# Optimization experiments

Measured on AMD Instinct MI355X. Metric: run time of the kernel, lower is better.

## Reference

```python
import jax, jax.numpy as jnp
import numpy as np

N_NODES = 50000
N_EDGES = 800000
DIM = 128
LAYERS = 3


def setup_inputs() -> dict:
    key = jax.random.key(0)
    k1, k2, k3, k4 = jax.random.split(key, 4)
    x = jax.random.normal(k1, (N_NODES, DIM), dtype=jnp.float32)
    edge_index = jax.random.randint(k2, (2, N_EDGES), 0, N_NODES, dtype=jnp.int64)
    scale = 1.0 / np.sqrt(DIM)
    W_rel = jax.random.normal(k3, (LAYERS, DIM, DIM), dtype=jnp.float32) * scale
    W_root = jax.random.normal(k4, (LAYERS, DIM, DIM), dtype=jnp.float32) * scale
    b = jnp.zeros((LAYERS, DIM), dtype=jnp.float32)
    return {"x": x, "edge_index": edge_index, "W_rel": W_rel, "W_root": W_root, "b": b}


def graph_conv(x, src, dst, w_rel, w_root, bias):
    # message: gather source node features along each edge  [E, D]
    msg = x[src]
    # add-aggregation per destination node                  [N, D]
    agg = jax.ops.segment_sum(msg, dst, num_segments=N_NODES)
    # out_i = W_rel @ agg_i + W_root @ x_i + b
    return agg @ w_rel + x @ w_root + bias


def reference(x, edge_index, W_rel, W_root, b):
    src, dst = edge_index[0], edge_index[1]
    for l in range(LAYERS):
        x = graph_conv(x, src, dst, W_rel[l], W_root[l], b[l])
    return x
```

## Files before the change

kernel.cpp:

```cpp
#include <hip/hip_runtime.h>

#define N_NODES 50000
#define N_EDGES 800000
#define DIM     128
#define LAYERS  3

#define BSHIFT    7
#define N_BUCKETS 391
#define CHUNK     4096
#define N_CHUNKS  196

using short8 = __attribute__((ext_vector_type(8))) short;
using f32x4  = __attribute__((ext_vector_type(4))) float;

__device__ __forceinline__ unsigned short f2bf(float f) {
    unsigned int u = __builtin_bit_cast(unsigned int, f);
    unsigned int r = (u + 0x7fffu + ((u >> 16) & 1u)) >> 16;
    return (unsigned short)r;
}
__device__ __forceinline__ float bfl(unsigned int u) {
    return __builtin_bit_cast(float, u << 16);
}
__device__ __forceinline__ float bfh(unsigned int u) {
    return __builtin_bit_cast(float, u & 0xffff0000u);
}


__global__ __launch_bounds__(256) void convert_x(const float* __restrict__ x,
                                                 unsigned short* __restrict__ xb) {
    int t = blockIdx.x * 256 + threadIdx.x;
    size_t base = (size_t)t * 8;
    if (base >= (size_t)N_NODES * DIM) return;
    float4 v0 = *(const float4*)(x + base);
    float4 v1 = *(const float4*)(x + base + 4);
    uint4 o;
    o.x = ((unsigned)f2bf(v0.y) << 16) | f2bf(v0.x);
    o.y = ((unsigned)f2bf(v0.w) << 16) | f2bf(v0.z);
    o.z = ((unsigned)f2bf(v1.y) << 16) | f2bf(v1.x);
    o.w = ((unsigned)f2bf(v1.w) << 16) | f2bf(v1.z);
    *(uint4*)(xb + base) = o;
}

__global__ __launch_bounds__(256) void prep_w(const float* __restrict__ Wrel,
                                              const float* __restrict__ Wroot,
                                              unsigned short* __restrict__ Wt) {
    int t = blockIdx.x * 256 + threadIdx.x;
    if (t >= LAYERS * 2 * 128 * 32) return;
    int k4  = t & 31;
    int col = (t >> 5) & 127;
    int mat = (t >> 12) & 1;
    int l   = t >> 13;
    const float* W = (mat ? Wroot : Wrel) + (size_t)l * DIM * DIM;
    int k0 = k4 * 4;
    unsigned short b0 = f2bf(W[(size_t)(k0 + 0) * DIM + col]);
    unsigned short b1 = f2bf(W[(size_t)(k0 + 1) * DIM + col]);
    unsigned short b2 = f2bf(W[(size_t)(k0 + 2) * DIM + col]);
    unsigned short b3 = f2bf(W[(size_t)(k0 + 3) * DIM + col]);
    uint2 o;
    o.x = ((unsigned)b1 << 16) | b0;
    o.y = ((unsigned)b3 << 16) | b2;
    *(uint2*)(Wt + (size_t)l * 128 * 256 + (size_t)col * 256 + mat * 128 + k0) = o;
}


__global__ __launch_bounds__(1024) void bin_count(const int* __restrict__ dst,
                                                  int* __restrict__ bcnt) {
    __shared__ int hist[N_BUCKETS];
    int tid = threadIdx.x, chunk = blockIdx.x;
    for (int t = tid; t < N_BUCKETS; t += 1024) hist[t] = 0;
    __syncthreads();
    int base = chunk * CHUNK;
#pragma unroll
    for (int i = 0; i < CHUNK; i += 1024) {
        int e = base + i + tid;
        if (e < N_EDGES) atomicAdd(&hist[dst[e] >> BSHIFT], 1);
    }
    __syncthreads();
    for (int t = tid; t < N_BUCKETS; t += 1024)
        bcnt[chunk * N_BUCKETS + t] = hist[t];
}

__global__ __launch_bounds__(512) void bscan(const int* __restrict__ bcnt,
                                             int* __restrict__ boff,
                                             int* __restrict__ bucket_start) {
    __shared__ int sh[512];
    int b = threadIdx.x;
    int run = 0;
    if (b < N_BUCKETS) {
        for (int c = 0; c < N_CHUNKS; ++c) {
            int v = bcnt[c * N_BUCKETS + b];
            boff[c * N_BUCKETS + b] = run;
            run += v;
        }
    }
    sh[b] = (b < N_BUCKETS) ? run : 0;
    __syncthreads();
    for (int off = 1; off < 512; off <<= 1) {
        int t = (b >= off) ? sh[b - off] : 0;
        __syncthreads();
        sh[b] += t;
        __syncthreads();
    }
    if (b < N_BUCKETS) bucket_start[b] = sh[b] - run;
    if (b == N_BUCKETS - 1) bucket_start[N_BUCKETS] = sh[b];
}

__global__ __launch_bounds__(1024) void bin_scatter(const int* __restrict__ src,
                                                    const int* __restrict__ dst,
                                                    const int* __restrict__ bucket_start,
                                                    const int* __restrict__ boff,
                                                    unsigned int* __restrict__ pairs) {
    __shared__ int cur[N_BUCKETS];
    int tid = threadIdx.x, chunk = blockIdx.x;
    for (int t = tid; t < N_BUCKETS; t += 1024)
        cur[t] = bucket_start[t] + boff[chunk * N_BUCKETS + t];
    __syncthreads();
    int base = chunk * CHUNK;
#pragma unroll
    for (int i = 0; i < CHUNK; i += 1024) {
        int e = base + i + tid;
        if (e < N_EDGES) {
            int d = dst[e];
            int b = d >> BSHIFT;
            int p = atomicAdd(&cur[b], 1);
            pairs[p] = ((unsigned)(d & 127) << 16) | (unsigned)src[e];
        }
    }
}

__global__ __launch_bounds__(1024) void fill_lds(const unsigned int* __restrict__ pairs,
                                                 const int* __restrict__ bucket_start,
                                                 int* __restrict__ row_start,
                                                 unsigned short* __restrict__ srcs16) {
    __shared__ int hist[128];
    __shared__ int offs[128];
    __shared__ int cur[128];
    __shared__ unsigned short srt[4096];
    int b = blockIdx.x, tid = threadIdx.x;
    int s0 = bucket_start[b], s1 = bucket_start[b + 1];
    int cnt = s1 - s0;
    if (tid < 128) hist[tid] = 0;
    __syncthreads();
    for (int k = tid; k < cnt; k += 1024)
        atomicAdd(&hist[pairs[s0 + k] >> 16], 1);
    __syncthreads();
    if (tid < 128) offs[tid] = hist[tid];
    __syncthreads();
    for (int off = 1; off < 128; off <<= 1) {
        int t = 0;
        if (tid < 128 && tid >= off) t = offs[tid - off];
        __syncthreads();
        if (tid < 128) offs[tid] += t;
        __syncthreads();
    }
    if (tid < 128) {
        int excl = offs[tid] - hist[tid];
        cur[tid] = excl;
        int node = b * 128 + tid;
        if (node <= N_NODES) row_start[node] = s0 + excl;
    }
    __syncthreads();
    for (int k = tid; k < cnt; k += 1024) {
        unsigned int u = pairs[s0 + k];
        int p = atomicAdd(&cur[u >> 16], 1);
        srt[p] = (unsigned short)(u & 0xffffu);
    }
    __syncthreads();
    for (int k = tid; k < cnt; k += 1024)
        srcs16[s0 + k] = srt[k];
}


__device__ __forceinline__ void acc8(float* a, uint4 v) {
    a[0] += bfl(v.x); a[1] += bfh(v.x);
    a[2] += bfl(v.y); a[3] += bfh(v.y);
    a[4] += bfl(v.z); a[5] += bfh(v.z);
    a[6] += bfl(v.w); a[7] += bfh(v.w);
}

__global__ __launch_bounds__(256) void aggregate_bf16(const unsigned short* __restrict__ xb,
                                                      const int* __restrict__ row_start,
                                                      const unsigned short* __restrict__ srcs,
                                                      unsigned short* __restrict__ aggb) {
    int tid  = threadIdx.x;
    int L    = tid & 15;
    int node = blockIdx.x * 16 + (tid >> 4);
    if (node >= N_NODES) return;
    int j   = row_start[node];
    int end = row_start[node + 1];

    const uint4* xq = (const uint4*)xb;
    float a[8] = {0.f, 0.f, 0.f, 0.f, 0.f, 0.f, 0.f, 0.f};

    for (; j + 7 < end; j += 8) {
        uint4 v0 = xq[(size_t)srcs[j]     * 16 + L];
        uint4 v1 = xq[(size_t)srcs[j + 1] * 16 + L];
        uint4 v2 = xq[(size_t)srcs[j + 2] * 16 + L];
        uint4 v3 = xq[(size_t)srcs[j + 3] * 16 + L];
        uint4 v4 = xq[(size_t)srcs[j + 4] * 16 + L];
        uint4 v5 = xq[(size_t)srcs[j + 5] * 16 + L];
        uint4 v6 = xq[(size_t)srcs[j + 6] * 16 + L];
        uint4 v7 = xq[(size_t)srcs[j + 7] * 16 + L];
        acc8(a, v0); acc8(a, v1); acc8(a, v2); acc8(a, v3);
        acc8(a, v4); acc8(a, v5); acc8(a, v6); acc8(a, v7);
    }
    if (j + 3 < end) {
        uint4 v0 = xq[(size_t)srcs[j]     * 16 + L];
        uint4 v1 = xq[(size_t)srcs[j + 1] * 16 + L];
        uint4 v2 = xq[(size_t)srcs[j + 2] * 16 + L];
        uint4 v3 = xq[(size_t)srcs[j + 3] * 16 + L];
        acc8(a, v0); acc8(a, v1); acc8(a, v2); acc8(a, v3);
        j += 4;
    }
    int rem = end - j;
    if (rem > 0) {
        int j1 = (rem > 1) ? j + 1 : j;
        int j2 = (rem > 2) ? j + 2 : j;
        uint4 v0 = xq[(size_t)srcs[j]  * 16 + L];
        uint4 v1 = xq[(size_t)srcs[j1] * 16 + L];
        uint4 v2 = xq[(size_t)srcs[j2] * 16 + L];
        acc8(a, v0);
        if (rem > 1) acc8(a, v1);
        if (rem > 2) acc8(a, v2);
    }

    uint4 o;
    o.x = ((unsigned)f2bf(a[1]) << 16) | f2bf(a[0]);
    o.y = ((unsigned)f2bf(a[3]) << 16) | f2bf(a[2]);
    o.z = ((unsigned)f2bf(a[5]) << 16) | f2bf(a[4]);
    o.w = ((unsigned)f2bf(a[7]) << 16) | f2bf(a[6]);
    ((uint4*)aggb)[(size_t)node * 16 + L] = o;
}


__global__ __launch_bounds__(256) void gemm_bf16(const unsigned short* __restrict__ aggb,
                                                 const unsigned short* __restrict__ xb,
                                                 const unsigned short* __restrict__ Wt_l,
                                                 const float* __restrict__ bias,
                                                 unsigned short* __restrict__ outb,
                                                 float* __restrict__ outf) {
    __shared__ unsigned short Bs[128 * 256];

    int tid  = threadIdx.x;
    int lane = tid & 63;
    int w    = tid >> 6;

#pragma unroll
    for (int i = 0; i < 16; ++i) {
        int c   = tid + i * 256;
        int col = c >> 5;
        int q   = c & 31;
        uint4 v = ((const uint4*)Wt_l)[c];
        *(uint4*)&Bs[col * 256 + 8 * (q ^ (col & 7))] = v;
    }
    __syncthreads();

    int row0 = blockIdx.x * 128 + w * 32;

    f32x4 acc[2][8];
#pragma unroll
    for (int m = 0; m < 2; ++m)
#pragma unroll
        for (int n = 0; n < 8; ++n) acc[m][n] = (f32x4){0.f, 0.f, 0.f, 0.f};

    const short8 zero8 = {0, 0, 0, 0, 0, 0, 0, 0};

#pragma unroll
    for (int ch = 0; ch < 8; ++ch) {
        const unsigned short* Asrc = (ch < 4) ? aggb : xb;
        int k0 = (ch & 3) * 32 + (lane >> 4) * 8;

        short8 a[2];
#pragma unroll
        for (int m = 0; m < 2; ++m) {
            int r = row0 + m * 16 + (lane & 15);
            a[m] = (r < N_NODES) ? *(const short8*)(Asrc + (size_t)r * DIM + k0) : zero8;
        }

        int qbase = ch * 4 + (lane >> 4);
#pragma unroll
        for (int n = 0; n < 8; ++n) {
            int col = n * 16 + (lane & 15);
            short8 b = *(const short8*)&Bs[col * 256 + 8 * (qbase ^ (col & 7))];
            acc[0][n] = __builtin_amdgcn_mfma_f32_16x16x32_bf16(a[0], b, acc[0][n], 0, 0, 0);
            acc[1][n] = __builtin_amdgcn_mfma_f32_16x16x32_bf16(a[1], b, acc[1][n], 0, 0, 0);
        }
    }

#pragma unroll
    for (int n = 0; n < 8; ++n) {
        int col = n * 16 + (lane & 15);
        float bv = bias[col];
#pragma unroll
        for (int m = 0; m < 2; ++m) {
            int rb = row0 + m * 16 + (lane >> 4) * 4;
#pragma unroll
            for (int r = 0; r < 4; ++r) {
                int row = rb + r;
                if (row < N_NODES) {
                    float v = acc[m][n][r] + bv;
                    if (outf) outf[(size_t)row * DIM + col] = v;
                    else      outb[(size_t)row * DIM + col] = f2bf(v);
                }
            }
        }
    }
}


extern "C" void kernel_launch(void* const* d_in, const int* in_sizes, int n_in,
                              void* d_out, int out_size, void* d_ws, size_t ws_size,
                              hipStream_t stream) {
    const float* x0    = (const float*)d_in[0];
    const int*   ei    = (const int*)d_in[1];
    const float* Wrel  = (const float*)d_in[2];
    const float* Wroot = (const float*)d_in[3];
    const float* bvec  = (const float*)d_in[4];
    float* out = (float*)d_out;

    char* ws = (char*)d_ws;
    const size_t XB = (size_t)N_NODES * DIM * sizeof(unsigned short);
    unsigned short* xbA  = (unsigned short*)ws;
    unsigned short* xbB  = (unsigned short*)(ws + XB);
    unsigned short* aggb = (unsigned short*)(ws + 2 * XB);
    unsigned int* pairs  = (unsigned int*)(ws + 2 * XB);
    int* bcnt            = (int*)(ws + 2 * XB + 3200000);
    int* boff            = (int*)(ws + 2 * XB + 3506944);
    int* bucket_start    = (int*)(ws + 2 * XB + 3813504);
    unsigned short* Wt   = (unsigned short*)(ws + 3 * XB);
    unsigned short* srcs16 = (unsigned short*)(ws + 3 * XB + 196608);
    int* row_start       = (int*)(ws + 3 * XB + 196608 + 1600000);

    const int* src = ei;
    const int* dst = ei + N_EDGES;

    convert_x<<<(N_NODES * DIM / 8 + 255) / 256, 256, 0, stream>>>(x0, xbA);
    prep_w<<<(LAYERS * 2 * 128 * 32 + 255) / 256, 256, 0, stream>>>(Wrel, Wroot, Wt);

    bin_count<<<N_CHUNKS, 1024, 0, stream>>>(dst, bcnt);
    bscan<<<1, 512, 0, stream>>>(bcnt, boff, bucket_start);
    bin_scatter<<<N_CHUNKS, 1024, 0, stream>>>(src, dst, bucket_start, boff, pairs);
    fill_lds<<<N_BUCKETS, 1024, 0, stream>>>(pairs, bucket_start, row_start, srcs16);

    unsigned short* xin = xbA;
    unsigned short* xouts[LAYERS] = {xbB, xbA, nullptr};
    for (int l = 0; l < LAYERS; ++l) {
        aggregate_bf16<<<(N_NODES + 15) / 16, 256, 0, stream>>>(xin, row_start, srcs16, aggb);
        gemm_bf16<<<(N_NODES + 127) / 128, 256, 0, stream>>>(
            aggb, xin, Wt + (size_t)l * 128 * 256, bvec + (size_t)l * DIM,
            xouts[l], (l == LAYERS - 1) ? out : nullptr);
        xin = xouts[l];
    }
}
```

Measured before the change: 243.6 us.

## Fuse neighbor aggregation and GEMM into one per-layer kernel

Merges the aggregate and GEMM kernels into a single kernel per layer. Each block of 64 nodes gathers neighbor sums into LDS and then runs MFMA directly from LDS, which removes the global write and re-read of the aggregated buffer and one launch per layer. Weights are pre-packed in MFMA fragment order and read straight from global/L2 instead of being staged in LDS. The trade-offs are lower per-block GEMM reuse (64 rows instead of 128), per-wave weight reloads from cache, and the block's MFMA phase waiting on its slowest node's gather.

Result: no change. 240.4 us (-1.3%).

```diff
diff --git a/kernel.cpp b/kernel.cpp
--- a/kernel.cpp
+++ b/kernel.cpp
@@ -9,6 +9,8 @@
 #define N_BUCKETS 391
 #define CHUNK     4096
 #define N_CHUNKS  196
+
+#define AS_STRIDE 136
 
 using short8 = __attribute__((ext_vector_type(8))) short;
 using f32x4  = __attribute__((ext_vector_type(4))) float;
@@ -41,25 +43,29 @@
     *(uint4*)(xb + base) = o;
 }
 
-__global__ __launch_bounds__(256) void prep_w(const float* __restrict__ Wrel,
-                                              const float* __restrict__ Wroot,
-                                              unsigned short* __restrict__ Wt) {
+__global__ __launch_bounds__(256) void prep_wf(const float* __restrict__ Wrel,
+                                               const float* __restrict__ Wroot,
+                                               unsigned short* __restrict__ Wf) {
     int t = blockIdx.x * 256 + threadIdx.x;
-    if (t >= LAYERS * 2 * 128 * 32) return;
-    int k4  = t & 31;
-    int col = (t >> 5) & 127;
-    int mat = (t >> 12) & 1;
-    int l   = t >> 13;
-    const float* W = (mat ? Wroot : Wrel) + (size_t)l * DIM * DIM;
-    int k0 = k4 * 4;
-    unsigned short b0 = f2bf(W[(size_t)(k0 + 0) * DIM + col]);
-    unsigned short b1 = f2bf(W[(size_t)(k0 + 1) * DIM + col]);
-    unsigned short b2 = f2bf(W[(size_t)(k0 + 2) * DIM + col]);
-    unsigned short b3 = f2bf(W[(size_t)(k0 + 3) * DIM + col]);
-    uint2 o;
-    o.x = ((unsigned)b1 << 16) | b0;
-    o.y = ((unsigned)b3 << 16) | b2;
-    *(uint2*)(Wt + (size_t)l * 128 * 256 + (size_t)col * 256 + mat * 128 + k0) = o;
+    if (t >= LAYERS * 4096) return;
+    int l    = t >> 12;
+    int rem  = t & 4095;
+    int f    = rem >> 6;
+    int lane = rem & 63;
+    int ch = f >> 3, n = f & 7;
+    int col = n * 16 + (lane & 15);
+    int ck0 = ch * 32 + ((lane >> 4) << 3);
+    const float* W = ((ck0 < 128) ? Wrel : Wroot) + (size_t)l * DIM * DIM;
+    int k0 = ck0 & 127;
+    unsigned short e[8];
+#pragma unroll
+    for (int i = 0; i < 8; ++i) e[i] = f2bf(W[(size_t)(k0 + i) * DIM + col]);
+    uint4 o;
+    o.x = ((unsigned)e[1] << 16) | e[0];
+    o.y = ((unsigned)e[3] << 16) | e[2];
+    o.z = ((unsigned)e[5] << 16) | e[4];
+    o.w = ((unsigned)e[7] << 16) | e[6];
+    *(uint4*)(Wf + (size_t)t * 8) = o;
 }
 
 
@@ -178,112 +184,90 @@
     a[6] += bfl(v.w); a[7] += bfh(v.w);
 }
 
-__global__ __launch_bounds__(256) void aggregate_bf16(const unsigned short* __restrict__ xb,
-                                                      const int* __restrict__ row_start,
-                                                      const unsigned short* __restrict__ srcs,
-                                                      unsigned short* __restrict__ aggb) {
-    int tid  = threadIdx.x;
-    int L    = tid & 15;
-    int node = blockIdx.x * 16 + (tid >> 4);
-    if (node >= N_NODES) return;
-    int j   = row_start[node];
-    int end = row_start[node + 1];
-
-    const uint4* xq = (const uint4*)xb;
-    float a[8] = {0.f, 0.f, 0.f, 0.f, 0.f, 0.f, 0.f, 0.f};
-
-    for (; j + 7 < end; j += 8) {
-        uint4 v0 = xq[(size_t)srcs[j]     * 16 + L];
-        uint4 v1 = xq[(size_t)srcs[j + 1] * 16 + L];
-        uint4 v2 = xq[(size_t)srcs[j + 2] * 16 + L];
-        uint4 v3 = xq[(size_t)srcs[j + 3] * 16 + L];
-        uint4 v4 = xq[(size_t)srcs[j + 4] * 16 + L];
-        uint4 v5 = xq[(size_t)srcs[j + 5] * 16 + L];
-        uint4 v6 = xq[(size_t)srcs[j + 6] * 16 + L];
-        uint4 v7 = xq[(size_t)srcs[j + 7] * 16 + L];
-        acc8(a, v0); acc8(a, v1); acc8(a, v2); acc8(a, v3);
-        acc8(a, v4); acc8(a, v5); acc8(a, v6); acc8(a, v7);
-    }
-    if (j + 3 < end) {
-        uint4 v0 = xq[(size_t)srcs[j]     * 16 + L];
-        uint4 v1 = xq[(size_t)srcs[j + 1] * 16 + L];
-        uint4 v2 = xq[(size_t)srcs[j + 2] * 16 + L];
-        uint4 v3 = xq[(size_t)srcs[j + 3] * 16 + L];
-        acc8(a, v0); acc8(a, v1); acc8(a, v2); acc8(a, v3);
-        j += 4;
-    }
-    int rem = end - j;
-    if (rem > 0) {
-        int j1 = (rem > 1) ? j + 1 : j;
-        int j2 = (rem > 2) ? j + 2 : j;
-        uint4 v0 = xq[(size_t)srcs[j]  * 16 + L];
-        uint4 v1 = xq[(size_t)srcs[j1] * 16 + L];
-        uint4 v2 = xq[(size_t)srcs[j2] * 16 + L];
-        acc8(a, v0);
-        if (rem > 1) acc8(a, v1);
-        if (rem > 2) acc8(a, v2);
-    }
-
-    uint4 o;
-    o.x = ((unsigned)f2bf(a[1]) << 16) | f2bf(a[0]);
-    o.y = ((unsigned)f2bf(a[3]) << 16) | f2bf(a[2]);
-    o.z = ((unsigned)f2bf(a[5]) << 16) | f2bf(a[4]);
-    o.w = ((unsigned)f2bf(a[7]) << 16) | f2bf(a[6]);
-    ((uint4*)aggb)[(size_t)node * 16 + L] = o;
-}
-
-
-__global__ __launch_bounds__(256) void gemm_bf16(const unsigned short* __restrict__ aggb,
-                                                 const unsigned short* __restrict__ xb,
-                                                 const unsigned short* __restrict__ Wt_l,
-                                                 const float* __restrict__ bias,
-                                                 unsigned short* __restrict__ outb,
-                                                 float* __restrict__ outf) {
-    __shared__ unsigned short Bs[128 * 256];
-
-    int tid  = threadIdx.x;
-    int lane = tid & 63;
-    int w    = tid >> 6;
-
-#pragma unroll
-    for (int i = 0; i < 16; ++i) {
-        int c   = tid + i * 256;
-        int col = c >> 5;
-        int q   = c & 31;
-        uint4 v = ((const uint4*)Wt_l)[c];
-        *(uint4*)&Bs[col * 256 + 8 * (q ^ (col & 7))] = v;
-    }
-    __syncthreads();
-
-    int row0 = blockIdx.x * 128 + w * 32;
-
-    f32x4 acc[2][8];
-#pragma unroll
-    for (int m = 0; m < 2; ++m)
-#pragma unroll
-        for (int n = 0; n < 8; ++n) acc[m][n] = (f32x4){0.f, 0.f, 0.f, 0.f};
+__global__ __launch_bounds__(256) void layer_fused(const unsigned short* __restrict__ xin,
+                                                   const int* __restrict__ row_start,
+                                                   const unsigned short* __restrict__ srcs,
+                                                   const unsigned short* __restrict__ Wf,
+                                                   const float* __restrict__ bias,
+                                                   unsigned short* __restrict__ outb,
+                                                   float* __restrict__ outf) {
+    __shared__ unsigned short As[64 * AS_STRIDE];
+
+    int tid = threadIdx.x;
+    const uint4* xq = (const uint4*)xin;
+
+    int L = tid & 15, grp = tid >> 4;
+#pragma unroll
+    for (int i = 0; i < 4; ++i) {
+        int local = grp * 4 + i;
+        int node = blockIdx.x * 64 + local;
+        float a[8] = {0.f, 0.f, 0.f, 0.f, 0.f, 0.f, 0.f, 0.f};
+        if (node < N_NODES) {
+            int j = row_start[node], end = row_start[node + 1];
+            for (; j + 7 < end; j += 8) {
+                uint4 v0 = xq[(size_t)srcs[j]     * 16 + L];
+                uint4 v1 = xq[(size_t)srcs[j + 1] * 16 + L];
+                uint4 v2 = xq[(size_t)srcs[j + 2] * 16 + L];
+                uint4 v3 = xq[(size_t)srcs[j + 3] * 16 + L];
+                uint4 v4 = xq[(size_t)srcs[j + 4] * 16 + L];
+                uint4 v5 = xq[(size_t)srcs[j + 5] * 16 + L];
+                uint4 v6 = xq[(size_t)srcs[j + 6] * 16 + L];
+                uint4 v7 = xq[(size_t)srcs[j + 7] * 16 + L];
+                acc8(a, v0); acc8(a, v1); acc8(a, v2); acc8(a, v3);
+                acc8(a, v4); acc8(a, v5); acc8(a, v6); acc8(a, v7);
+            }
+            if (j + 3 < end) {
+                uint4 v0 = xq[(size_t)srcs[j]     * 16 + L];
+                uint4 v1 = xq[(size_t)srcs[j + 1] * 16 + L];
+                uint4 v2 = xq[(size_t)srcs[j + 2] * 16 + L];
+                uint4 v3 = xq[(size_t)srcs[j + 3] * 16 + L];
+                acc8(a, v0); acc8(a, v1); acc8(a, v2); acc8(a, v3);
+                j += 4;
+            }
+            int rem = end - j;
+            if (rem > 0) {
+                int j1 = (rem > 1) ? j + 1 : j;
+                int j2 = (rem > 2) ? j + 2 : j;
+                uint4 v0 = xq[(size_t)srcs[j]  * 16 + L];
+                uint4 v1 = xq[(size_t)srcs[j1] * 16 + L];
+                uint4 v2 = xq[(size_t)srcs[j2] * 16 + L];
+                acc8(a, v0);
+                if (rem > 1) acc8(a, v1);
+                if (rem > 2) acc8(a, v2);
+            }
+        }
+        uint4 o;
+        o.x = ((unsigned)f2bf(a[1]) << 16) | f2bf(a[0]);
+        o.y = ((unsigned)f2bf(a[3]) << 16) | f2bf(a[2]);
+        o.z = ((unsigned)f2bf(a[5]) << 16) | f2bf(a[4]);
+        o.w = ((unsigned)f2bf(a[7]) << 16) | f2bf(a[6]);
+        *(uint4*)&As[local * AS_STRIDE + L * 8] = o;
+    }
+    __syncthreads();
+
+    int lane = tid & 63, w = tid >> 6;
+    int rloc = w * 16 + (lane & 15);
+
+    f32x4 acc[8];
+#pragma unroll
+    for (int n = 0; n < 8; ++n) acc[n] = (f32x4){0.f, 0.f, 0.f, 0.f};
 
     const short8 zero8 = {0, 0, 0, 0, 0, 0, 0, 0};
 
 #pragma unroll
     for (int ch = 0; ch < 8; ++ch) {
-        const unsigned short* Asrc = (ch < 4) ? aggb : xb;
-        int k0 = (ch & 3) * 32 + (lane >> 4) * 8;
-
-        short8 a[2];
-#pragma unroll
-        for (int m = 0; m < 2; ++m) {
-            int r = row0 + m * 16 + (lane & 15);
-            a[m] = (r < N_NODES) ? *(const short8*)(Asrc + (size_t)r * DIM + k0) : zero8;
-        }
-
-        int qbase = ch * 4 + (lane >> 4);
+        short8 a;
+        if (ch < 4) {
+            a = *(const short8*)&As[rloc * AS_STRIDE + ch * 32 + (lane >> 4) * 8];
+        } else {
+            int r = blockIdx.x * 64 + rloc;
+            int k0 = (ch - 4) * 32 + (lane >> 4) * 8;
+            a = (r < N_NODES) ? *(const short8*)(xin + (size_t)r * DIM + k0) : zero8;
+        }
 #pragma unroll
         for (int n = 0; n < 8; ++n) {
-            int col = n * 16 + (lane & 15);
-            short8 b = *(const short8*)&Bs[col * 256 + 8 * (qbase ^ (col & 7))];
-            acc[0][n] = __builtin_amdgcn_mfma_f32_16x16x32_bf16(a[0], b, acc[0][n], 0, 0, 0);
-            acc[1][n] = __builtin_amdgcn_mfma_f32_16x16x32_bf16(a[1], b, acc[1][n], 0, 0, 0);
+            short8 b = *(const short8*)(Wf + ((size_t)(ch * 8 + n) * 64 + lane) * 8);
+            acc[n] = __builtin_amdgcn_mfma_f32_16x16x32_bf16(a, b, acc[n], 0, 0, 0);
         }
     }
 
@@ -291,17 +275,14 @@
     for (int n = 0; n < 8; ++n) {
         int col = n * 16 + (lane & 15);
         float bv = bias[col];
-#pragma unroll
-        for (int m = 0; m < 2; ++m) {
-            int rb = row0 + m * 16 + (lane >> 4) * 4;
-#pragma unroll
-            for (int r = 0; r < 4; ++r) {
-                int row = rb + r;
-                if (row < N_NODES) {
-                    float v = acc[m][n][r] + bv;
-                    if (outf) outf[(size_t)row * DIM + col] = v;
-                    else      outb[(size_t)row * DIM + col] = f2bf(v);
-                }
+        int rb = blockIdx.x * 64 + w * 16 + (lane >> 4) * 4;
+#pragma unroll
+        for (int r = 0; r < 4; ++r) {
+            int row = rb + r;
+            if (row < N_NODES) {
+                float v = acc[n][r] + bv;
+                if (outf) outf[(size_t)row * DIM + col] = v;
+                else      outb[(size_t)row * DIM + col] = f2bf(v);
             }
         }
     }
@@ -322,12 +303,11 @@
     const size_t XB = (size_t)N_NODES * DIM * sizeof(unsigned short);
     unsigned short* xbA  = (unsigned short*)ws;
     unsigned short* xbB  = (unsigned short*)(ws + XB);
-    unsigned short* aggb = (unsigned short*)(ws + 2 * XB);
     unsigned int* pairs  = (unsigned int*)(ws + 2 * XB);
     int* bcnt            = (int*)(ws + 2 * XB + 3200000);
     int* boff            = (int*)(ws + 2 * XB + 3506944);
     int* bucket_start    = (int*)(ws + 2 * XB + 3813504);
-    unsigned short* Wt   = (unsigned short*)(ws + 3 * XB);
+    unsigned short* Wf   = (unsigned short*)(ws + 3 * XB);
     unsigned short* srcs16 = (unsigned short*)(ws + 3 * XB + 196608);
     int* row_start       = (int*)(ws + 3 * XB + 196608 + 1600000);
 
@@ -335,7 +315,7 @@
     const int* dst = ei + N_EDGES;
 
     convert_x<<<(N_NODES * DIM / 8 + 255) / 256, 256, 0, stream>>>(x0, xbA);
-    prep_w<<<(LAYERS * 2 * 128 * 32 + 255) / 256, 256, 0, stream>>>(Wrel, Wroot, Wt);
+    prep_wf<<<(LAYERS * 4096 + 255) / 256, 256, 0, stream>>>(Wrel, Wroot, Wf);
 
     bin_count<<<N_CHUNKS, 1024, 0, stream>>>(dst, bcnt);
     bscan<<<1, 512, 0, stream>>>(bcnt, boff, bucket_start);
@@ -344,10 +324,10 @@
 
     unsigned short* xin = xbA;
     unsigned short* xouts[LAYERS] = {xbB, xbA, nullptr};
+    const int GRID = (N_NODES + 63) / 64;
     for (int l = 0; l < LAYERS; ++l) {
-        aggregate_bf16<<<(N_NODES + 15) / 16, 256, 0, stream>>>(xin, row_start, srcs16, aggb);
-        gemm_bf16<<<(N_NODES + 127) / 128, 256, 0, stream>>>(
-            aggb, xin, Wt + (size_t)l * 128 * 256, bvec + (size_t)l * DIM,
+        layer_fused<<<GRID, 256, 0, stream>>>(
+            xin, row_start, srcs16, Wf + (size_t)l * 32768, bvec + (size_t)l * DIM,
             xouts[l], (l == LAYERS - 1) ? out : nullptr);
         xin = xouts[l];
     }
```
